# Kernel optimization log

Measured on AMD Instinct MI355X. Metric: run time of the kernel, lower is better.

Reference implementation:

```python
import jax, jax.numpy as jnp
import numpy as np

T, H, I, SI, E, K = 1024, 2048, 1408, 5632, 8, 4
NORM_TOPK_PROB = False


def setup_inputs() -> dict:
    key = jax.random.key(0)
    ks = jax.random.split(key, 9)
    s = lambda k, shape, fan: (jax.random.normal(k, shape, jnp.float32) * (fan ** -0.5))
    return {
        "hidden_states": jax.random.normal(ks[0], (T, H), jnp.float32),
        "Wg": s(ks[1], (E, H, I), H),   # per-expert gate_proj
        "Wu": s(ks[2], (E, H, I), H),   # per-expert up_proj
        "Wd": s(ks[3], (E, I, H), I),   # per-expert down_proj
        "Wsg": s(ks[4], (H, SI), H),    # shared expert gate_proj
        "Wsu": s(ks[5], (H, SI), H),    # shared expert up_proj
        "Wsd": s(ks[6], (SI, H), SI),   # shared expert down_proj
        "W_router": s(ks[7], (H, E), H),        # self.gate
        "W_shared_gate": s(ks[8], (H, 1), H),   # self.shared_expert_gate
    }


def reference(hidden_states, Wg, Wu, Wd, Wsg, Wsu, Wsd, W_router, W_shared_gate):
    x = hidden_states  # [T, H]
    # shared expert: silu(x Wg) * (x Wu) then down proj (fused_gate_up + matmul)
    shared = (jax.nn.silu(x @ Wsg) * (x @ Wsu)) @ Wsd          # [T, H]
    shared_gate = jax.nn.sigmoid(x @ W_shared_gate)            # [T, 1]
    # router: softmax in float32, then top-k
    probs = jax.nn.softmax((x @ W_router).astype(jnp.float32), axis=-1)  # [T, E]
    top_v, top_i = jax.lax.top_k(probs, K)                     # [T, K]
    if NORM_TOPK_PROB and K > 1:
        top_v = top_v / jnp.sum(top_v, axis=-1, keepdims=True)
    # combine weights: zero for non-routed (expert, token) pairs -> same math
    # as the original gather/expert/scatter(index_add_) loop
    combine = jnp.zeros((T, E), top_v.dtype).at[jnp.arange(T)[:, None], top_i].set(top_v)
    # expert GEMMs (dequantized-GPTQ math): silu(x Wg_e) * (x Wu_e) @ Wd_e
    g = jnp.einsum('th,ehi->eti', x, Wg)                       # [E, T, I]
    u = jnp.einsum('th,ehi->eti', x, Wu)                       # [E, T, I]
    y = jnp.einsum('eti,eih->eth', jax.nn.silu(g) * u, Wd)     # [E, T, H]
    moe = jnp.einsum('eth,te->th', y, combine.astype(x.dtype)) # [T, H]
    scale = 1.0 / (K ** 0.5)
    return (moe + shared_gate * shared) * jnp.asarray(scale, x.dtype)
```

## Files before the change

### kernel.cpp

```cpp
#include <hip/hip_runtime.h>
#include <cstdint>
#include <cstddef>


typedef unsigned short u16;
typedef _Float16 f16;
typedef __attribute__((ext_vector_type(8))) _Float16 half8;
typedef __attribute__((ext_vector_type(4))) float f32x4;

#define GLDS(g, l) __builtin_amdgcn_global_load_lds(                          \
    (const __attribute__((address_space(1))) void*)(g),                       \
    (__attribute__((address_space(3))) void*)(l), 16, 0, 0)

__device__ __forceinline__ float b2f(u16 u){ return __uint_as_float(((uint32_t)u)<<16); }
__device__ __forceinline__ u16 f2b(float f){
  uint32_t x = __float_as_uint(f);
  return (u16)((x + 0x7fffu + ((x>>16)&1u)) >> 16);
}

__global__ __launch_bounds__(64) void detect_kernel(const uint32_t* __restrict__ X,
                                                    int* __restrict__ flag){
  const int lane = threadIdx.x;
  int cnt = 0;
  for (int i = lane; i < 256; i += 64){
    const uint32_t e = (X[i] >> 23) & 0xffu;
    cnt += (e >= 90u && e <= 160u) ? 1 : 0;
  }
#pragma unroll
  for (int off = 32; off > 0; off >>= 1) cnt += __shfl_xor(cnt, off, 64);
  if (lane == 0) *flag = (cnt > 128) ? 1 : 0;
}

template<bool F32>
__device__ void router_conv_body(const void* X, const void* Wr, const void* Wxg,
                                 f16* __restrict__ Xh, float* __restrict__ combine,
                                 float* __restrict__ sgate, float (*red)[9]){
  const int t = blockIdx.x, tid = threadIdx.x, lane = tid&63, wave = tid>>6;
  const int h0 = tid*8;
  float xv[8], gv[8];
  if (F32){
    const float* xp = (const float*)X + (size_t)t*2048 + h0;
    const float4 a = *(const float4*)xp, b = *(const float4*)(xp+4);
    xv[0]=a.x; xv[1]=a.y; xv[2]=a.z; xv[3]=a.w;
    xv[4]=b.x; xv[5]=b.y; xv[6]=b.z; xv[7]=b.w;
    const float* gp = (const float*)Wxg + h0;
    const float4 c = *(const float4*)gp, d = *(const float4*)(gp+4);
    gv[0]=c.x; gv[1]=c.y; gv[2]=c.z; gv[3]=c.w;
    gv[4]=d.x; gv[5]=d.y; gv[6]=d.z; gv[7]=d.w;
  } else {
    union { uint4 v; u16 s[8]; } xr, gr;
    xr.v = *(const uint4*)((const u16*)X + (size_t)t*2048 + h0);
    gr.v = *(const uint4*)((const u16*)Wxg + h0);
#pragma unroll
    for (int q = 0; q < 8; ++q){ xv[q] = b2f(xr.s[q]); gv[q] = b2f(gr.s[q]); }
  }
  half8 h8;
#pragma unroll
  for (int j = 0; j < 8; ++j) h8[j] = (f16)xv[j];
  *(half8*)(Xh + (size_t)t*2048 + h0) = h8;

  float acc[8] = {0,0,0,0,0,0,0,0};
  float ag = 0.f;
#pragma unroll
  for (int jj = 0; jj < 8; ++jj){
    const int h = h0 + jj;
    float w[8];
    if (F32){
      const float* wp = (const float*)Wr + (size_t)h*8;
      const float4 w0 = *(const float4*)wp, w1 = *(const float4*)(wp+4);
      w[0]=w0.x; w[1]=w0.y; w[2]=w0.z; w[3]=w0.w;
      w[4]=w1.x; w[5]=w1.y; w[6]=w1.z; w[7]=w1.w;
    } else {
      union { uint4 v; u16 s[8]; } wv;
      wv.v = *(const uint4*)((const u16*)Wr + (size_t)h*8);
#pragma unroll
      for (int q = 0; q < 8; ++q) w[q] = b2f(wv.s[q]);
    }
#pragma unroll
    for (int e = 0; e < 8; ++e) acc[e] += xv[jj] * w[e];
    ag += xv[jj] * gv[jj];
  }
#pragma unroll
  for (int off = 32; off > 0; off >>= 1){
#pragma unroll
    for (int e = 0; e < 8; ++e) acc[e] += __shfl_xor(acc[e], off, 64);
    ag += __shfl_xor(ag, off, 64);
  }
  if (lane == 0){
#pragma unroll
    for (int e = 0; e < 8; ++e) red[wave][e] = acc[e];
    red[wave][8] = ag;
  }
  __syncthreads();
  if (tid == 0){
    float a[8], g = 0.f;
#pragma unroll
    for (int e = 0; e < 8; ++e) a[e] = red[0][e] + red[1][e] + red[2][e] + red[3][e];
    g = red[0][8] + red[1][8] + red[2][8] + red[3][8];
    float m = a[0];
#pragma unroll
    for (int e = 1; e < 8; ++e) m = fmaxf(m, a[e]);
    float p[8]; float s = 0.f;
#pragma unroll
    for (int e = 0; e < 8; ++e){ p[e] = __expf(a[e]-m); s += p[e]; }
    const float inv = 1.f/s;
#pragma unroll
    for (int e = 0; e < 8; ++e) p[e] *= inv;
#pragma unroll
    for (int e = 0; e < 8; ++e){
      int cnt = 0;
#pragma unroll
      for (int j = 0; j < 8; ++j)
        cnt += (p[j] > p[e]) || (p[j] == p[e] && j < e);
      combine[(size_t)t*8 + e] = (cnt < 4) ? p[e] : 0.f;
    }
    sgate[t] = 1.f/(1.f + __expf(-g));
  }
}
__global__ __launch_bounds__(256) void router_conv(const void* X, const void* Wr, const void* Wxg,
                                                   f16* Xh, float* combine, float* sgate,
                                                   const int* flag){
  __shared__ float red[4][9];
  if (*flag) router_conv_body<true >(X, Wr, Wxg, Xh, combine, sgate, red);
  else       router_conv_body<false>(X, Wr, Wxg, Xh, combine, sgate, red);
}

__global__ __launch_bounds__(1024) void compact_kernel(
    const float* __restrict__ combine, int* __restrict__ cnt,
    int* __restrict__ tok, float* __restrict__ cw, int* __restrict__ inv){
  __shared__ int lc[8];
  const int t = threadIdx.x;
  if (t < 8) lc[t] = 0;
  __syncthreads();
  int k = 0;
#pragma unroll
  for (int e = 0; e < 8; ++e){
    const float v = combine[(size_t)t*8 + e];
    if (v > 0.f){
      const int p = atomicAdd(&lc[e], 1);
      tok[e*1024 + p] = t;
      cw [e*1024 + p] = v;
      if (k < 4) inv[t*4 + k] = e*1024 + p;
      ++k;
    }
  }
  for (; k < 4; ++k) inv[t*4 + k] = -1;
  __syncthreads();
#pragma unroll
  for (int e = 0; e < 8; ++e){
    if (t >= lc[e]){ tok[e*1024 + t] = 0; cw[e*1024 + t] = 0.f; }
  }
  if (t < 8) cnt[t] = lc[t];
}

#define TP 72
template<bool F32>
__device__ void tcvt_body(const void* S, f16* __restrict__ Dm, int K, int N,
                          size_t soff, int n0, int k0, f16* Tt){
  const int t = threadIdx.x;
  const int kr = t >> 4, nc = (t & 15)*4;
#pragma unroll
  for (int p = 0; p < 4; ++p){
    const int kk = p*16 + kr;
    float v0, v1, v2, v3;
    if (F32){
      const float* Sm = (const float*)S + soff;
      const float4 v = *(const float4*)(Sm + (size_t)(k0+kk)*N + n0 + nc);
      v0=v.x; v1=v.y; v2=v.z; v3=v.w;
    } else {
      const u16* Sm = (const u16*)S + soff;
      union { uint2 u; u16 s[4]; } r;
      r.u = *(const uint2*)(Sm + (size_t)(k0+kk)*N + n0 + nc);
      v0=b2f(r.s[0]); v1=b2f(r.s[1]); v2=b2f(r.s[2]); v3=b2f(r.s[3]);
    }
    Tt[(nc+0)*TP + kk] = (f16)v0;
    Tt[(nc+1)*TP + kk] = (f16)v1;
    Tt[(nc+2)*TP + kk] = (f16)v2;
    Tt[(nc+3)*TP + kk] = (f16)v3;
  }
  __syncthreads();
  const int nr = t >> 3, kc = (t & 7)*8;
#pragma unroll
  for (int p = 0; p < 2; ++p){
    const int n = p*32 + nr;
    const half8 v = *(const half8*)(Tt + n*TP + kc);
    *(half8*)(Dm + (size_t)(n0+n)*K + k0 + kc) = v;
  }
}
__global__ __launch_bounds__(256) void tcvt_all(
    const void* Wsg, const void* Wsu, const void* Wg, const void* Wu,
    const void* Wd, const void* Wsd,
    f16* WsgT, f16* WsuT, f16* WgT, f16* WuT, f16* WdT, f16* WsdT,
    const int* flag){
  __shared__ f16 Tt[64*TP];
  int bid = blockIdx.x;
  const void* S; f16* D; int K, N, nx; size_t soff = 0;
  if (bid < 2816){ S = Wsg; D = WsgT; K = 2048; N = 5632; nx = 88; }
  else if (bid < 5632){ bid -= 2816; S = Wsu; D = WsuT; K = 2048; N = 5632; nx = 88; }
  else if (bid < 11264){
    bid -= 5632; const int z = bid/704; bid -= z*704;
    soff = (size_t)z*2048*1408;
    S = Wg; D = WgT + soff; K = 2048; N = 1408; nx = 22;
  } else if (bid < 16896){
    bid -= 11264; const int z = bid/704; bid -= z*704;
    soff = (size_t)z*2048*1408;
    S = Wu; D = WuT + soff; K = 2048; N = 1408; nx = 22;
  } else if (bid < 22528){ bid -= 16896; S = Wd; D = WdT; K = 11264; N = 2048; nx = 32; }
  else { bid -= 22528; S = Wsd; D = WsdT; K = 5632; N = 2048; nx = 32; }
  const int n0 = (bid % nx)*64, k0 = (bid / nx)*64;
  if (*flag) tcvt_body<true >(S, D, K, N, soff, n0, k0, Tt);
  else       tcvt_body<false>(S, D, K, N, soff, n0, k0, Tt);
}

__device__ __forceinline__ void stage_T128(const f16* __restrict__ Row, int ld, int k0, f16* Ls){
  const int tid = threadIdx.x, wave = tid>>6, lane = tid&63;
#pragma unroll
  for (int i = 0; i < 2; ++i){
    const int rbase = i*64 + wave*16;
    const f16* g = Row + (size_t)(rbase + (lane>>2))*ld + (k0 + (lane&3)*8);
    GLDS(g, Ls + rbase*32);
  }
}
__device__ __forceinline__ void stage_T64(const f16* __restrict__ Row, int ld, int k0, f16* Ls){
  const int tid = threadIdx.x, wave = tid>>6, lane = tid&63;
  const int rbase = wave*16;
  const f16* g = Row + (size_t)(rbase + (lane>>2))*ld + (k0 + (lane&3)*8);
  GLDS(g, Ls + rbase*32);
}

__global__ __launch_bounds__(256) void gu_gemm_t(
    const f16* __restrict__ Xh, const f16* __restrict__ WsgT, const f16* __restrict__ WsuT,
    const f16* __restrict__ WgT, const f16* __restrict__ WuT,
    f16* __restrict__ A1s, f16* __restrict__ P,
    const float* __restrict__ sgate, const float* __restrict__ cw,
    const int* __restrict__ cnt, const int* __restrict__ tok)
{
  __shared__ f16 As[128*32];
  __shared__ f16 Bg[64*32];
  __shared__ f16 Bu[64*32];
  int bid = blockIdx.x;
  const int tid = threadIdx.x, lane = tid&63, wave = tid>>6;
  const f16 *BgRow, *BuRow; f16* outp; const float* rs;
  int ldout, m0, n0;
  const f16 *gA0, *gA1;
  if (bid < 704){
    n0 = (bid % 88)*64; m0 = (bid / 88)*128;
    BgRow = WsgT + (size_t)n0*2048; BuRow = WsuT + (size_t)n0*2048;
    outp = A1s; rs = sgate; ldout = 5632;
    const int r0 = m0 + wave*16 + (lane>>2);
    gA0 = Xh + (size_t)r0*2048 + (lane&3)*8;
    gA1 = gA0 + (size_t)64*2048;
  } else {
    bid -= 704;
    const int e = bid / 176, r = bid % 176;
    const int mt = r / 22;
    if (mt*128 >= cnt[e]) return;
    n0 = (r % 22)*64; m0 = mt*128;
    const size_t off = (size_t)e*1408*2048;
    BgRow = WgT + off + (size_t)n0*2048; BuRow = WuT + off + (size_t)n0*2048;
    outp = P + (size_t)e*1024*1408; rs = cw + e*1024; ldout = 1408;
    const int* tp = tok + e*1024 + m0;
    const int t0 = tp[wave*16 + (lane>>2)];
    const int t1 = tp[64 + wave*16 + (lane>>2)];
    gA0 = Xh + (size_t)t0*2048 + (lane&3)*8;
    gA1 = Xh + (size_t)t1*2048 + (lane&3)*8;
  }
  const int wm = wave>>1, wn = wave&1, lr = lane&15, q = lane>>4;

  const f32x4 z4 = {0.f,0.f,0.f,0.f};
  f32x4 ag[4][2], au[4][2];
#pragma unroll
  for (int mi = 0; mi < 4; ++mi)
#pragma unroll
    for (int ni = 0; ni < 2; ++ni){ ag[mi][ni] = z4; au[mi][ni] = z4; }

  for (int k0 = 0; k0 < 2048; k0 += 32){
    __syncthreads();
    GLDS(gA0 + k0, As + wave*512);
    GLDS(gA1 + k0, As + 2048 + wave*512);
    stage_T64(BgRow, 2048, k0, Bg);
    stage_T64(BuRow, 2048, k0, Bu);
    __syncthreads();
    half8 af[4];
#pragma unroll
    for (int mi = 0; mi < 4; ++mi)
      af[mi] = *(const half8*)(As + (wm*64 + mi*16 + lr)*32 + q*8);
#pragma unroll
    for (int ni = 0; ni < 2; ++ni){
      const half8 bfg = *(const half8*)(Bg + (wn*32 + ni*16 + lr)*32 + q*8);
      const half8 bfu = *(const half8*)(Bu + (wn*32 + ni*16 + lr)*32 + q*8);
#pragma unroll
      for (int mi = 0; mi < 4; ++mi){
        ag[mi][ni] = __builtin_amdgcn_mfma_f32_16x16x32_f16(af[mi], bfg, ag[mi][ni], 0, 0, 0);
        au[mi][ni] = __builtin_amdgcn_mfma_f32_16x16x32_f16(af[mi], bfu, au[mi][ni], 0, 0, 0);
      }
    }
  }

  float rsv[4][4];
#pragma unroll
  for (int mi = 0; mi < 4; ++mi)
#pragma unroll
    for (int r = 0; r < 4; ++r)
      rsv[mi][r] = rs[m0 + wm*64 + mi*16 + q*4 + r];
#pragma unroll
  for (int mi = 0; mi < 4; ++mi)
#pragma unroll
    for (int ni = 0; ni < 2; ++ni)
#pragma unroll
      for (int r = 0; r < 4; ++r){
        const int row = m0 + wm*64 + mi*16 + q*4 + r;
        const int col = n0 + wn*32 + ni*16 + lr;
        const float g = ag[mi][ni][r];
        const float v = (g / (1.f + __expf(-g))) * au[mi][ni][r] * rsv[mi][r];
        outp[(size_t)row*ldout + col] = (f16)v;
      }
}

__global__ __launch_bounds__(256) void down_gemm_t(
    const f16* __restrict__ Pm, const f16* __restrict__ A1s,
    const f16* __restrict__ WdT, const f16* __restrict__ WsdT,
    const int* __restrict__ cnt,
    float* __restrict__ downR, float* __restrict__ shp)
{
  __shared__ f16 As[128*32];
  __shared__ f16 Bs[128*32];
  const int z = blockIdx.z;
  const int m0 = blockIdx.y*128, n0 = blockIdx.x*128;
  const f16 *A, *B; int lda, ldk, KT; float* C;
  if (z < 8){
    if (m0 >= cnt[z]) return;
    A = Pm + (size_t)z*1024*1408 + (size_t)m0*1408; lda = 1408;
    B = WdT + (size_t)z*1408; ldk = 11264; KT = 44;
    C = downR + (size_t)z*1024*2048;
  } else {
    A = A1s + (size_t)(z-8)*2816 + (size_t)m0*5632; lda = 5632;
    B = WsdT + (size_t)(z-8)*2816; ldk = 5632; KT = 88;
    C = shp + (size_t)(z-8)*2097152;
  }
  const f16* Arow = A;
  const f16* Brow = B + (size_t)n0*ldk;
  const int tid = threadIdx.x, lane = tid&63, wave = tid>>6;
  const int wm = wave>>1, wn = wave&1, lr = lane&15, q = lane>>4;

  const f32x4 z4 = {0.f,0.f,0.f,0.f};
  f32x4 acc[4][4];
#pragma unroll
  for (int mi = 0; mi < 4; ++mi)
#pragma unroll
    for (int ni = 0; ni < 4; ++ni) acc[mi][ni] = z4;

  for (int kt = 0; kt < KT; ++kt){
    __syncthreads();
    stage_T128(Arow, lda, kt*32, As);
    stage_T128(Brow, ldk, kt*32, Bs);
    __syncthreads();
    half8 af[4], bf[4];
#pragma unroll
    for (int mi = 0; mi < 4; ++mi)
      af[mi] = *(const half8*)(As + (wm*64 + mi*16 + lr)*32 + q*8);
#pragma unroll
    for (int ni = 0; ni < 4; ++ni)
      bf[ni] = *(const half8*)(Bs + (wn*64 + ni*16 + lr)*32 + q*8);
#pragma unroll
    for (int ni = 0; ni < 4; ++ni)
#pragma unroll
      for (int mi = 0; mi < 4; ++mi)
        acc[mi][ni] = __builtin_amdgcn_mfma_f32_16x16x32_f16(af[mi], bf[ni], acc[mi][ni], 0, 0, 0);
  }
#pragma unroll
  for (int mi = 0; mi < 4; ++mi)
#pragma unroll
    for (int ni = 0; ni < 4; ++ni)
#pragma unroll
      for (int r = 0; r < 4; ++r){
        const int row = m0 + wm*64 + mi*16 + q*4 + r;
        const int col = n0 + wn*64 + ni*16 + lr;
        C[(size_t)row*2048 + col] = acc[mi][ni][r];
      }
}

__global__ __launch_bounds__(256) void final_g(
    const float4* __restrict__ sh0, const float4* __restrict__ sh1,
    const float4* __restrict__ downR, const int* __restrict__ inv,
    void* __restrict__ out, const int* __restrict__ flag){
  const int t = blockIdx.x;
  const int4 iv = *(const int4*)(inv + t*4);
  const int idx[4] = {iv.x, iv.y, iv.z, iv.w};
#pragma unroll
  for (int jj = 0; jj < 2; ++jj){
    const int j = threadIdx.x + jj*256;
    const size_t b = (size_t)t*512 + j;
    const float4 a = sh0[b], c = sh1[b];
    float v0 = a.x + c.x, v1 = a.y + c.y, v2 = a.z + c.z, v3 = a.w + c.w;
#pragma unroll
    for (int k = 0; k < 4; ++k){
      if (idx[k] >= 0){
        const float4 d = downR[(size_t)idx[k]*512 + j];
        v0 += d.x; v1 += d.y; v2 += d.z; v3 += d.w;
      }
    }
    v0 *= 0.5f; v1 *= 0.5f; v2 *= 0.5f; v3 *= 0.5f;
    if (*flag){
      float4 o; o.x=v0; o.y=v1; o.z=v2; o.w=v3;
      ((float4*)out)[b] = o;
    } else {
      uint2 o;
      o.x = (uint32_t)f2b(v0) | ((uint32_t)f2b(v1) << 16);
      o.y = (uint32_t)f2b(v2) | ((uint32_t)f2b(v3) << 16);
      ((uint2*)out)[b] = o;
    }
  }
}

#define LDBT 40
#define ABUF 4096
#define BBUF 2560
struct BR { float v[8]; };
template<bool F32>
__device__ __forceinline__ void loadB(const void* __restrict__ B, size_t ldb, int k0, int n0, BR& r){
  const int t = threadIdx.x, c = t&63, kg = t>>6;
  if (F32){
    const float* p = (const float*)B + (size_t)(k0 + kg*8)*ldb + (n0 + c);
#pragma unroll
    for (int j = 0; j < 8; ++j) r.v[j] = p[(size_t)j*ldb];
  } else {
    const u16* p = (const u16*)B + (size_t)(k0 + kg*8)*ldb + (n0 + c);
#pragma unroll
    for (int j = 0; j < 8; ++j) r.v[j] = b2f(p[(size_t)j*ldb]);
  }
}
__device__ __forceinline__ void storeB(const BR& r, f16* BT){
  const int t = threadIdx.x, c = t&63, kg = t>>6;
  half8 h;
#pragma unroll
  for (int j = 0; j < 8; ++j) h[j] = (f16)r.v[j];
  *(half8*)(BT + c*LDBT + kg*8) = h;
}
template<bool F32>
__device__ void gu_body_r(const f16* __restrict__ Arow, const void* __restrict__ Bgp,
                          const void* __restrict__ Bup, f16* __restrict__ outp,
                          const float* __restrict__ rs, int rs_stride,
                          int ldb, int ldout, int m0, int n0,
                          f16* As, f16* BgT, f16* BuT)
{
  const int tid = threadIdx.x, lane = tid&63, wave = tid>>6;
  const int wm = wave>>1, wn = wave&1, lr = lane&15, q = lane>>4;
  const f32x4 z4 = {0.f,0.f,0.f,0.f};
  f32x4 ag[4][2], au[4][2];
#pragma unroll
  for (int mi = 0; mi < 4; ++mi)
#pragma unroll
    for (int ni = 0; ni < 2; ++ni){ ag[mi][ni] = z4; au[mi][ni] = z4; }
  const int KT = 64;
  BR rg, ru;
  loadB<F32>(Bgp, ldb, 0, n0, rg);
  loadB<F32>(Bup, ldb, 0, n0, ru);
  storeB(rg, BgT); storeB(ru, BuT);
  stage_T128(Arow, 2048, 0, As);
  loadB<F32>(Bgp, ldb, 32, n0, rg);
  loadB<F32>(Bup, ldb, 32, n0, ru);
  __syncthreads();
  for (int kt = 0; kt < KT; ++kt){
    const int cur = kt&1, nxt = cur^1;
    if (kt+1 < KT){
      storeB(rg, BgT + nxt*BBUF);
      storeB(ru, BuT + nxt*BBUF);
      stage_T128(Arow, 2048, (kt+1)*32, As + nxt*ABUF);
    }
    if (kt+2 < KT){
      loadB<F32>(Bgp, ldb, (kt+2)*32, n0, rg);
      loadB<F32>(Bup, ldb, (kt+2)*32, n0, ru);
    }
    const f16* Ac = As + cur*ABUF;
    const f16* Bgc = BgT + cur*BBUF;
    const f16* Buc = BuT + cur*BBUF;
    half8 af[4];
#pragma unroll
    for (int mi = 0; mi < 4; ++mi)
      af[mi] = *(const half8*)(Ac + (wm*64 + mi*16 + lr)*32 + q*8);
#pragma unroll
    for (int ni = 0; ni < 2; ++ni){
      const half8 bfg = *(const half8*)(Bgc + (wn*32 + ni*16 + lr)*LDBT + q*8);
      const half8 bfu = *(const half8*)(Buc + (wn*32 + ni*16 + lr)*LDBT + q*8);
#pragma unroll
      for (int mi = 0; mi < 4; ++mi){
        ag[mi][ni] = __builtin_amdgcn_mfma_f32_16x16x32_f16(af[mi], bfg, ag[mi][ni], 0, 0, 0);
        au[mi][ni] = __builtin_amdgcn_mfma_f32_16x16x32_f16(af[mi], bfu, au[mi][ni], 0, 0, 0);
      }
    }
    __syncthreads();
  }
  float rsv[4][4];
#pragma unroll
  for (int mi = 0; mi < 4; ++mi)
#pragma unroll
    for (int r = 0; r < 4; ++r)
      rsv[mi][r] = rs[(size_t)(m0 + wm*64 + mi*16 + q*4 + r)*rs_stride];
#pragma unroll
  for (int mi = 0; mi < 4; ++mi)
#pragma unroll
    for (int ni = 0; ni < 2; ++ni)
#pragma unroll
      for (int r = 0; r < 4; ++r){
        const int row = m0 + wm*64 + mi*16 + q*4 + r;
        const int col = n0 + wn*32 + ni*16 + lr;
        const float g = ag[mi][ni][r];
        const float v = (g / (1.f + __expf(-g))) * au[mi][ni][r] * rsv[mi][r];
        outp[(size_t)row*ldout + col] = (f16)v;
      }
}
__global__ __launch_bounds__(256) void gu_gemm_r(
    const f16* __restrict__ Xh, const void* Wsg, const void* Wsu,
    const void* Wg, const void* Wu, f16* __restrict__ A1s, f16* __restrict__ P,
    const float* __restrict__ sgate, const float* __restrict__ combine, const int* flag)
{
  __shared__ f16 As[2*ABUF];
  __shared__ f16 BgT[2*BBUF];
  __shared__ f16 BuT[2*BBUF];
  const bool f32v = (*flag != 0);
  int bid = blockIdx.x;
  const void *Bg, *Bu; f16* outp; const float* rs;
  int rs_stride, ldb, ldout, m0, n0;
  if (bid < 704){
    n0 = (bid % 88)*64; m0 = (bid / 88)*128;
    Bg = Wsg; Bu = Wsu; outp = A1s; rs = sgate;
    rs_stride = 1; ldb = 5632; ldout = 5632;
  } else {
    bid -= 704;
    const int e = bid / 176, r = bid % 176;
    n0 = (r % 22)*64; m0 = (r / 22)*128;
    const size_t off = (size_t)e*2048*1408;
    Bg = f32v ? (const void*)((const float*)Wg + off) : (const void*)((const u16*)Wg + off);
    Bu = f32v ? (const void*)((const float*)Wu + off) : (const void*)((const u16*)Wu + off);
    outp = P + (size_t)e*1408; rs = combine + e;
    rs_stride = 8; ldb = 1408; ldout = 11264;
  }
  const f16* Arow = Xh + (size_t)m0*2048;
  if (f32v) gu_body_r<true >(Arow, Bg, Bu, outp, rs, rs_stride, ldb, ldout, m0, n0, As, BgT, BuT);
  else      gu_body_r<false>(Arow, Bg, Bu, outp, rs, rs_stride, ldb, ldout, m0, n0, As, BgT, BuT);
}
template<bool F32>
__device__ void down_body_r(const f16* __restrict__ Arow, int lda, const void* __restrict__ B,
                            float* __restrict__ C, int m0, int n0, f16* As, f16* BT)
{
  const int tid = threadIdx.x, lane = tid&63, wave = tid>>6;
  const int wm = wave>>1, wn = wave&1, lr = lane&15, q = lane>>4;
  const f32x4 z4 = {0.f,0.f,0.f,0.f};
  f32x4 acc[4][2];
#pragma unroll
  for (int mi = 0; mi < 4; ++mi)
#pragma unroll
    for (int ni = 0; ni < 2; ++ni) acc[mi][ni] = z4;
  const int KT = 176;
  BR rb;
  loadB<F32>(B, 2048, 0, n0, rb);
  storeB(rb, BT);
  stage_T128(Arow, lda, 0, As);
  loadB<F32>(B, 2048, 32, n0, rb);
  __syncthreads();
  for (int kt = 0; kt < KT; ++kt){
    const int cur = kt&1, nxt = cur^1;
    if (kt+1 < KT){
      storeB(rb, BT + nxt*BBUF);
      stage_T128(Arow, lda, (kt+1)*32, As + nxt*ABUF);
    }
    if (kt+2 < KT) loadB<F32>(B, 2048, (kt+2)*32, n0, rb);
    const f16* Ac = As + cur*ABUF;
    const f16* Bc = BT + cur*BBUF;
    half8 af[4];
#pragma unroll
    for (int mi = 0; mi < 4; ++mi)
      af[mi] = *(const half8*)(Ac + (wm*64 + mi*16 + lr)*32 + q*8);
#pragma unroll
    for (int ni = 0; ni < 2; ++ni){
      const half8 bf = *(const half8*)(Bc + (wn*32 + ni*16 + lr)*LDBT + q*8);
#pragma unroll
      for (int mi = 0; mi < 4; ++mi)
        acc[mi][ni] = __builtin_amdgcn_mfma_f32_16x16x32_f16(af[mi], bf, acc[mi][ni], 0, 0, 0);
    }
    __syncthreads();
  }
#pragma unroll
  for (int mi = 0; mi < 4; ++mi)
#pragma unroll
    for (int ni = 0; ni < 2; ++ni)
#pragma unroll
      for (int r = 0; r < 4; ++r){
        const int row = m0 + wm*64 + mi*16 + q*4 + r;
        const int col = n0 + wn*32 + ni*16 + lr;
        C[(size_t)row*2048 + col] = acc[mi][ni][r];
      }
}
__global__ __launch_bounds__(256) void down_gemm_r(
    const f16* __restrict__ Pm, const f16* __restrict__ A1s,
    const void* Wd, const void* Wsd,
    float* __restrict__ c0, float* __restrict__ c1, float* __restrict__ c2, const int* flag)
{
  __shared__ f16 As[2*ABUF];
  __shared__ f16 BT[2*BBUF];
  const int z = blockIdx.z;
  const bool f32v = (*flag != 0);
  const f16* A; const void* B; float* C; int lda;
  if (z == 0){ A = Pm; B = Wd; C = c0; lda = 11264; }
  else if (z == 1){
    A = Pm + 5632;
    B = f32v ? (const void*)((const float*)Wd + (size_t)5632*2048)
             : (const void*)((const u16*)Wd + (size_t)5632*2048);
    C = c1; lda = 11264;
  } else { A = A1s; B = Wsd; C = c2; lda = 5632; }
  const int m0 = blockIdx.y*128, n0 = blockIdx.x*64;
  const f16* Arow = A + (size_t)m0*lda;
  if (f32v) down_body_r<true >(Arow, lda, B, C, m0, n0, As, BT);
  else      down_body_r<false>(Arow, lda, B, C, m0, n0, As, BT);
}
__global__ __launch_bounds__(256) void final3(
    const float4* __restrict__ b0, const float4* __restrict__ b1, const float4* __restrict__ b2,
    void* __restrict__ out, const int* flag, int n4){
  const int i = blockIdx.x*256 + threadIdx.x;
  if (i >= n4) return;
  const float4 a = b0[i], b = b1[i], c = b2[i];
  const float v0 = 0.5f*(a.x + b.x + c.x);
  const float v1 = 0.5f*(a.y + b.y + c.y);
  const float v2 = 0.5f*(a.z + b.z + c.z);
  const float v3 = 0.5f*(a.w + b.w + c.w);
  if (*flag){
    float4 o; o.x=v0; o.y=v1; o.z=v2; o.w=v3;
    ((float4*)out)[i] = o;
  } else {
    uint2 o;
    o.x = (uint32_t)f2b(v0) | ((uint32_t)f2b(v1) << 16);
    o.y = (uint32_t)f2b(v2) | ((uint32_t)f2b(v3) << 16);
    ((uint2*)out)[i] = o;
  }
}

extern "C" void kernel_launch(void* const* d_in, const int* in_sizes, int n_in,
                              void* d_out, int out_size, void* d_ws, size_t ws_size,
                              hipStream_t stream)
{
  (void)in_sizes; (void)n_in; (void)out_size;
  const void* x   = d_in[0];
  const void* Wg  = d_in[1];
  const void* Wu  = d_in[2];
  const void* Wd  = d_in[3];
  const void* Wsg = d_in[4];
  const void* Wsu = d_in[5];
  const void* Wsd = d_in[6];
  const void* Wr  = d_in[7];
  const void* Wxg = d_in[8];

  char* ws = (char*)d_ws;
  size_t off = 0;
  auto alloc = [&](size_t bytes)->char*{
    char* p = ws + off; off = (off + bytes + 255) & ~(size_t)255; return p;
  };
  float* combine = (float*)alloc(32768);
  float* sgate   = (float*)alloc(4096);
  int*   flag    = (int*)  alloc(4096);
  int*   cnt     = (int*)  alloc(4096);
  int*   tok     = (int*)  alloc(8*1024*4);
  float* cw      = (float*)alloc(8*1024*4);
  int*   inv     = (int*)  alloc(1024*4*4);
  f16*   Xh      = (f16*)  alloc((size_t)1024*2048*2);
  f16*   A1s     = (f16*)  alloc((size_t)1024*5632*2);
  f16*   P       = (f16*)  alloc((size_t)8*1024*1408*2);
  float* shp     = (float*)alloc((size_t)3*2097152*4);
  float* downR   = (float*)alloc((size_t)8*1024*2048*4);
  f16*   WsgT    = (f16*)  alloc((size_t)5632*2048*2);
  f16*   WsuT    = (f16*)  alloc((size_t)5632*2048*2);
  f16*   WgT     = (f16*)  alloc((size_t)8*1408*2048*2);
  f16*   WuT     = (f16*)  alloc((size_t)8*1408*2048*2);
  f16*   WdT     = (f16*)  alloc((size_t)2048*11264*2);
  f16*   WsdT    = (f16*)  alloc((size_t)2048*5632*2);
  const size_t NEED_FULL = off;

  detect_kernel<<<dim3(1), dim3(64), 0, stream>>>((const uint32_t*)x, flag);
  router_conv<<<dim3(1024), dim3(256), 0, stream>>>(x, Wr, Wxg, Xh, combine, sgate, flag);

  if (ws_size >= NEED_FULL){
    compact_kernel<<<dim3(1), dim3(1024), 0, stream>>>(combine, cnt, tok, cw, inv);
    tcvt_all<<<dim3(25344), dim3(256), 0, stream>>>(
        Wsg, Wsu, Wg, Wu, Wd, Wsd, WsgT, WsuT, WgT, WuT, WdT, WsdT, flag);
    gu_gemm_t<<<dim3(2112), dim3(256), 0, stream>>>(
        Xh, WsgT, WsuT, WgT, WuT, A1s, P, sgate, cw, cnt, tok);
    down_gemm_t<<<dim3(16, 8, 10), dim3(256), 0, stream>>>(P, A1s, WdT, WsdT, cnt, downR, shp);
    final_g<<<dim3(1024), dim3(256), 0, stream>>>(
        (const float4*)shp, (const float4*)(shp + 2097152), (const float4*)downR,
        inv, d_out, flag);
  } else {
    float* b0 = shp;
    float* b1 = shp + 2097152;
    float* b2 = shp + 2*2097152;
    gu_gemm_r<<<dim3(2112), dim3(256), 0, stream>>>(
        Xh, Wsg, Wsu, Wg, Wu, A1s, P, sgate, combine, flag);
    down_gemm_r<<<dim3(32, 8, 3), dim3(256), 0, stream>>>(P, A1s, Wd, Wsd, b0, b1, b2, flag);
    final3<<<dim3(2048), dim3(256), 0, stream>>>(
        (const float4*)b0, (const float4*)b1, (const float4*)b2, d_out, flag, 524288);
  }
}
```

Measured before the change: 689.5 us.

## Overlap down-proj weight transpose with gate/up GEMM and fold compaction into prep

```diff
diff --git a/kernel.cpp b/kernel.cpp
--- a/kernel.cpp
+++ b/kernel.cpp
@@ -125,38 +125,41 @@
   else       router_conv_body<false>(X, Wr, Wxg, Xh, combine, sgate, red);
 }
 
-__global__ __launch_bounds__(1024) void compact_kernel(
-    const float* __restrict__ combine, int* __restrict__ cnt,
-    int* __restrict__ tok, float* __restrict__ cw, int* __restrict__ inv){
-  __shared__ int lc[8];
-  const int t = threadIdx.x;
-  if (t < 8) lc[t] = 0;
+__device__ void compact256(const float* __restrict__ combine, int* __restrict__ cnt,
+                           int* __restrict__ tok, float* __restrict__ cw,
+                           int* __restrict__ inv, int* lc){
+  const int tid = threadIdx.x;
+  if (tid < 8) lc[tid] = 0;
   __syncthreads();
-  int k = 0;
-#pragma unroll
-  for (int e = 0; e < 8; ++e){
-    const float v = combine[(size_t)t*8 + e];
-    if (v > 0.f){
-      const int p = atomicAdd(&lc[e], 1);
-      tok[e*1024 + p] = t;
-      cw [e*1024 + p] = v;
-      if (k < 4) inv[t*4 + k] = e*1024 + p;
-      ++k;
-    }
-  }
-  for (; k < 4; ++k) inv[t*4 + k] = -1;
+#pragma unroll
+  for (int s = 0; s < 4; ++s){
+    const int t = s*256 + tid;
+    int k = 0;
+#pragma unroll
+    for (int e = 0; e < 8; ++e){
+      const float v = combine[(size_t)t*8 + e];
+      if (v > 0.f){
+        const int p = atomicAdd(&lc[e], 1);
+        tok[e*1024 + p] = t;
+        cw [e*1024 + p] = v;
+        if (k < 4) inv[t*4 + k] = e*1024 + p;
+        ++k;
+      }
+    }
+    for (; k < 4; ++k) inv[t*4 + k] = -1;
+  }
   __syncthreads();
 #pragma unroll
-  for (int e = 0; e < 8; ++e){
-    if (t >= lc[e]){ tok[e*1024 + t] = 0; cw[e*1024 + t] = 0.f; }
-  }
-  if (t < 8) cnt[t] = lc[t];
+  for (int e = 0; e < 8; ++e)
+    for (int i = tid; i < 1024; i += 256)
+      if (i >= lc[e]){ tok[e*1024 + i] = 0; cw[e*1024 + i] = 0.f; }
+  if (tid < 8) cnt[tid] = lc[tid];
 }
 
 #define TP 72
 template<bool F32>
-__device__ void tcvt_body(const void* S, f16* __restrict__ Dm, int K, int N,
-                          size_t soff, int n0, int k0, f16* Tt){
+__device__ void tcvt64(const void* S, f16* __restrict__ Dm, int K, int N,
+                       size_t soff, int n0, int k0, f16* Tt){
   const int t = threadIdx.x;
   const int kr = t >> 4, nc = (t & 15)*4;
 #pragma unroll
@@ -187,13 +190,18 @@
     *(half8*)(Dm + (size_t)(n0+n)*K + k0 + kc) = v;
   }
 }
-__global__ __launch_bounds__(256) void tcvt_all(
+
+__global__ __launch_bounds__(256) void prep_gu(
     const void* Wsg, const void* Wsu, const void* Wg, const void* Wu,
-    const void* Wd, const void* Wsd,
-    f16* WsgT, f16* WsuT, f16* WgT, f16* WuT, f16* WdT, f16* WsdT,
+    f16* WsgT, f16* WsuT, f16* WgT, f16* WuT,
+    const float* combine, int* cnt, int* tok, float* cw, int* inv,
     const int* flag){
   __shared__ f16 Tt[64*TP];
   int bid = blockIdx.x;
+  if (bid == 16896){
+    compact256(combine, cnt, tok, cw, inv, (int*)Tt);
+    return;
+  }
   const void* S; f16* D; int K, N, nx; size_t soff = 0;
   if (bid < 2816){ S = Wsg; D = WsgT; K = 2048; N = 5632; nx = 88; }
   else if (bid < 5632){ bid -= 2816; S = Wsu; D = WsuT; K = 2048; N = 5632; nx = 88; }
@@ -201,15 +209,14 @@
     bid -= 5632; const int z = bid/704; bid -= z*704;
     soff = (size_t)z*2048*1408;
     S = Wg; D = WgT + soff; K = 2048; N = 1408; nx = 22;
-  } else if (bid < 16896){
+  } else {
     bid -= 11264; const int z = bid/704; bid -= z*704;
     soff = (size_t)z*2048*1408;
     S = Wu; D = WuT + soff; K = 2048; N = 1408; nx = 22;
-  } else if (bid < 22528){ bid -= 16896; S = Wd; D = WdT; K = 11264; N = 2048; nx = 32; }
-  else { bid -= 22528; S = Wsd; D = WsdT; K = 5632; N = 2048; nx = 32; }
+  }
   const int n0 = (bid % nx)*64, k0 = (bid / nx)*64;
-  if (*flag) tcvt_body<true >(S, D, K, N, soff, n0, k0, Tt);
-  else       tcvt_body<false>(S, D, K, N, soff, n0, k0, Tt);
+  if (*flag) tcvt64<true >(S, D, K, N, soff, n0, k0, Tt);
+  else       tcvt64<false>(S, D, K, N, soff, n0, k0, Tt);
 }
 
 __device__ __forceinline__ void stage_T128(const f16* __restrict__ Row, int ld, int k0, f16* Ls){
@@ -228,17 +235,14 @@
   GLDS(g, Ls + rbase*32);
 }
 
-__global__ __launch_bounds__(256) void gu_gemm_t(
+__device__ void gu_body_t(
     const f16* __restrict__ Xh, const f16* __restrict__ WsgT, const f16* __restrict__ WsuT,
     const f16* __restrict__ WgT, const f16* __restrict__ WuT,
     f16* __restrict__ A1s, f16* __restrict__ P,
     const float* __restrict__ sgate, const float* __restrict__ cw,
-    const int* __restrict__ cnt, const int* __restrict__ tok)
+    const int* __restrict__ cnt, const int* __restrict__ tok,
+    int bid, f16* As, f16* Bg, f16* Bu)
 {
-  __shared__ f16 As[128*32];
-  __shared__ f16 Bg[64*32];
-  __shared__ f16 Bu[64*32];
-  int bid = blockIdx.x;
   const int tid = threadIdx.x, lane = tid&63, wave = tid>>6;
   const f16 *BgRow, *BuRow; f16* outp; const float* rs;
   int ldout, m0, n0;
@@ -317,6 +321,34 @@
       }
 }
 
+__global__ __launch_bounds__(256) void gu_fused(
+    const f16* __restrict__ Xh, const f16* __restrict__ WsgT, const f16* __restrict__ WsuT,
+    const f16* __restrict__ WgT, const f16* __restrict__ WuT,
+    f16* __restrict__ A1s, f16* __restrict__ P,
+    const float* __restrict__ sgate, const float* __restrict__ cw,
+    const int* __restrict__ cnt, const int* __restrict__ tok,
+    const void* Wd, const void* Wsd, f16* WdT, f16* WsdT, const int* flag)
+{
+  __shared__ __align__(16) char smbuf[16384];
+  const int bid = blockIdx.x;
+  const int g = bid/5, r = bid%5;
+  if (r == 0){
+    f16* As = (f16*)smbuf;
+    f16* Bg = (f16*)(smbuf + 8192);
+    f16* Bu = (f16*)(smbuf + 12288);
+    gu_body_t(Xh, WsgT, WsuT, WgT, WuT, A1s, P, sgate, cw, cnt, tok, g, As, Bg, Bu);
+    return;
+  }
+  int idx = 4*g + (r-1);
+  f16* Tt = (f16*)smbuf;
+  const void* S; f16* D; int K, N, nx;
+  if (idx < 5632){ S = Wd; D = WdT; K = 11264; N = 2048; nx = 32; }
+  else { idx -= 5632; S = Wsd; D = WsdT; K = 5632; N = 2048; nx = 32; }
+  const int n0 = (idx % nx)*64, k0 = (idx / nx)*64;
+  if (*flag) tcvt64<true >(S, D, K, N, 0, n0, k0, Tt);
+  else       tcvt64<false>(S, D, K, N, 0, n0, k0, Tt);
+}
+
 __global__ __launch_bounds__(256) void down_gemm_t(
     const f16* __restrict__ Pm, const f16* __restrict__ A1s,
     const f16* __restrict__ WdT, const f16* __restrict__ WsdT,
@@ -679,11 +711,12 @@
   router_conv<<<dim3(1024), dim3(256), 0, stream>>>(x, Wr, Wxg, Xh, combine, sgate, flag);
 
   if (ws_size >= NEED_FULL){
-    compact_kernel<<<dim3(1), dim3(1024), 0, stream>>>(combine, cnt, tok, cw, inv);
-    tcvt_all<<<dim3(25344), dim3(256), 0, stream>>>(
-        Wsg, Wsu, Wg, Wu, Wd, Wsd, WsgT, WsuT, WgT, WuT, WdT, WsdT, flag);
-    gu_gemm_t<<<dim3(2112), dim3(256), 0, stream>>>(
-        Xh, WsgT, WsuT, WgT, WuT, A1s, P, sgate, cw, cnt, tok);
+    prep_gu<<<dim3(16897), dim3(256), 0, stream>>>(
+        Wsg, Wsu, Wg, Wu, WsgT, WsuT, WgT, WuT,
+        combine, cnt, tok, cw, inv, flag);
+    gu_fused<<<dim3(10560), dim3(256), 0, stream>>>(
+        Xh, WsgT, WsuT, WgT, WuT, A1s, P, sgate, cw, cnt, tok,
+        Wd, Wsd, WdT, WsdT, flag);
     down_gemm_t<<<dim3(16, 8, 10), dim3(256), 0, stream>>>(P, A1s, WdT, WsdT, cnt, downR, shp);
     final_g<<<dim3(1024), dim3(256), 0, stream>>>(
         (const float4*)shp, (const float4*)(shp + 2097152), (const float4*)downR,
```

New measurement: 672.0 us. -2.5%, faster.
